# Kernel optimization log

Measured on AMD Instinct MI355X. Metric: run time of the kernel, lower is better.

## Reference

```python
import jax, jax.numpy as jnp
import numpy as np

NUM_TOKENS = 16384
DIM = 4096
N_EXPERTS = 256
ROUTE_SCALE = 1.0


def setup_inputs() -> dict:
    key = jax.random.key(0)
    k_x, k_w = jax.random.split(key)
    x = jax.random.normal(k_x, (NUM_TOKENS, DIM), dtype=jnp.float32)
    # nn.init.normal_(weight, std=0.02)
    weight = 0.02 * jax.random.normal(k_w, (N_EXPERTS, DIM), dtype=jnp.float32)
    return {"x": x, "weight": weight}


def reference(x, weight):
    # Router GEMM: [T, D] @ [D, E] -> [T, E]
    scores = jnp.einsum("td,ed->te", x, weight)
    # Eval-mode token_choice path: softmax in fp32
    probs = jax.nn.softmax(scores.astype(jnp.float32), axis=-1)  # [T, E]
    indices = jnp.argmax(probs, axis=-1, keepdims=True)  # [T, 1] int
    # Hard one-hot scatter of argmax
    y_hard = jax.nn.one_hot(indices[:, 0], N_EXPERTS, dtype=probs.dtype)  # [T, E]
    # Straight-through estimator mix
    ste = jax.lax.stop_gradient(y_hard - probs) + probs
    # Gather routing weight at the selected expert
    weights = jnp.take_along_axis(ste, indices, axis=-1)  # [T, 1]
    weights = (weights * ROUTE_SCALE).astype(x.dtype)
    return weights, indices
```

## Files before the change

### kernel.cpp

```cpp
#include <hip/hip_runtime.h>
#include <stdint.h>

#define NUM_TOKENS 16384
#define DIM        4096
#define NEXP       256
#define MB         32
#define BK         64
#define NITER      (DIM / BK)
#define APAD       72
#define NWAVES     8
#define MARGIN     0.025f
#define CAP        16384

typedef __attribute__((ext_vector_type(4))) float   f32x4;
typedef __attribute__((ext_vector_type(8))) __bf16  bf16x8;

static __device__ __forceinline__ unsigned short f32_to_bf16(float f) {
    unsigned int u = __float_as_uint(f);
    u += 0x7fffu + ((u >> 16) & 1u);
    return (unsigned short)(u >> 16);
}

__global__ void cvt_weights(const float* __restrict__ w,
                            unsigned short* __restrict__ wh,
                            int* __restrict__ counter) {
    if (blockIdx.x == 0 && threadIdx.x == 0) *counter = 0;
    const int n4 = NEXP * DIM / 4;
    const int stride = gridDim.x * blockDim.x;
    for (int i = blockIdx.x * blockDim.x + threadIdx.x; i < n4; i += stride) {
        float4 v = ((const float4*)w)[i];
        ushort4 h;
        h.x = f32_to_bf16(v.x); h.y = f32_to_bf16(v.y);
        h.z = f32_to_bf16(v.z); h.w = f32_to_bf16(v.w);
        ((ushort4*)wh)[i] = h;
    }
}

__global__ __launch_bounds__(512, 4) void gate_main(
    const float* __restrict__ x,
    const unsigned short* __restrict__ wh,
    float* __restrict__ out,
    int* __restrict__ counter,
    int4* __restrict__ entries)
{
    __shared__ unsigned short lAh[2][MB][APAD];
    __shared__ float4 cand[NWAVES][MB];

    const int tid  = threadIdx.x;
    const int wv   = tid >> 6;
    const int lane = tid & 63;
    const int tok0 = blockIdx.x * MB;

    const int ta   = tid >> 4;
    const int kcol = (tid & 15) * 4;
    const float* xrow = x + (size_t)(tok0 + ta) * DIM + kcol;

    const int quad = lane >> 4;
    const int col  = lane & 15;

    const unsigned short* bp[2];
    #pragma unroll
    for (int nt = 0; nt < 2; ++nt)
        bp[nt] = wh + (size_t)(wv * 32 + nt * 16 + col) * DIM + quad * 8;

    f32x4 acc[2][2];
    #pragma unroll
    for (int mt = 0; mt < 2; ++mt)
        #pragma unroll
        for (int nt = 0; nt < 2; ++nt)
            acc[mt][nt] = f32x4{0.f, 0.f, 0.f, 0.f};

    bf16x8 b[2][2];

    float4 xva = *(const float4*)(xrow);
    float4 xvb = *(const float4*)(xrow + BK);
    #pragma unroll
    for (int kk2 = 0; kk2 < 2; ++kk2)
        #pragma unroll
        for (int nt = 0; nt < 2; ++nt)
            b[kk2][nt] = *(const bf16x8*)(bp[nt] + kk2 * 32);
    {
        ushort4 h;
        h.x = f32_to_bf16(xva.x); h.y = f32_to_bf16(xva.y);
        h.z = f32_to_bf16(xva.z); h.w = f32_to_bf16(xva.w);
        *(ushort4*)&lAh[0][ta][kcol] = h;
    }
    xva = *(const float4*)(xrow + 2 * BK);

    asm volatile("s_waitcnt lgkmcnt(0)" ::: "memory");
    __builtin_amdgcn_s_barrier();
    asm volatile("" ::: "memory");

    auto iter_body = [&](int it, int cur, float4& xcons) {
        const int nxt = cur ^ 1;
        if (it + 1 < NITER) {
            ushort4 h;
            h.x = f32_to_bf16(xcons.x); h.y = f32_to_bf16(xcons.y);
            h.z = f32_to_bf16(xcons.z); h.w = f32_to_bf16(xcons.w);
            *(ushort4*)&lAh[nxt][ta][kcol] = h;
            if (it + 3 < NITER)
                xcons = *(const float4*)(xrow + (it + 3) * BK);
        }
        #pragma unroll
        for (int kk2 = 0; kk2 < 2; ++kk2) {
            bf16x8 ah0 = *(const bf16x8*)&lAh[cur][col][kk2 * 32 + quad * 8];
            bf16x8 ah1 = *(const bf16x8*)&lAh[cur][16 + col][kk2 * 32 + quad * 8];
            acc[0][0] = __builtin_amdgcn_mfma_f32_16x16x32_bf16(ah0, b[kk2][0], acc[0][0], 0, 0, 0);
            acc[1][0] = __builtin_amdgcn_mfma_f32_16x16x32_bf16(ah1, b[kk2][0], acc[1][0], 0, 0, 0);
            acc[0][1] = __builtin_amdgcn_mfma_f32_16x16x32_bf16(ah0, b[kk2][1], acc[0][1], 0, 0, 0);
            acc[1][1] = __builtin_amdgcn_mfma_f32_16x16x32_bf16(ah1, b[kk2][1], acc[1][1], 0, 0, 0);
            if (it + 1 < NITER) {
                #pragma unroll
                for (int nt = 0; nt < 2; ++nt)
                    b[kk2][nt] = *(const bf16x8*)(bp[nt] + (it + 1) * BK + kk2 * 32);
            }
        }
        asm volatile("s_waitcnt lgkmcnt(0)" ::: "memory");
        __builtin_amdgcn_s_barrier();
        asm volatile("" ::: "memory");
    };

    #pragma unroll 1
    for (int itp = 0; itp < NITER; itp += 2) {
        iter_body(itp,     0, xvb);
        iter_body(itp + 1, 1, xva);
    }

    #pragma unroll
    for (int mt = 0; mt < 2; ++mt) {
        #pragma unroll
        for (int r = 0; r < 4; ++r) {
            float s0 = acc[mt][0][r]; int e0 = wv * 32 + col;
            float s1 = acc[mt][1][r]; int e1 = e0 + 16;
            float t1s, t2s; int t1e, t2e;
            if (s1 > s0) { t1s = s1; t1e = e1; t2s = s0; t2e = e0; }
            else         { t1s = s0; t1e = e0; t2s = s1; t2e = e1; }
            #pragma unroll
            for (int m = 1; m <= 8; m <<= 1) {
                float o1s = __shfl_xor(t1s, m); int o1e = __shfl_xor(t1e, m);
                float o2s = __shfl_xor(t2s, m); int o2e = __shfl_xor(t2e, m);
                bool o1_top = (o1s > t1s) || (o1s == t1s && o1e < t1e);
                if (o1_top) {
                    bool keep_t1 = (t1s > o2s) || (t1s == o2s && t1e < o2e);
                    t2s = keep_t1 ? t1s : o2s; t2e = keep_t1 ? t1e : o2e;
                    t1s = o1s; t1e = o1e;
                } else {
                    bool o1_2nd = (o1s > t2s) || (o1s == t2s && o1e < t2e);
                    if (o1_2nd) { t2s = o1s; t2e = o1e; }
                }
            }
            if (col == 0) {
                int tok = mt * 16 + quad * 4 + r;
                cand[wv][tok] = make_float4(t1s, __int_as_float(t1e), t2s, __int_as_float(t2e));
            }
        }
    }
    __syncthreads();

    if (tid < MB) {
        float4 c0 = cand[0][tid];
        float t1s = c0.x; int t1e = __float_as_int(c0.y);
        float t2s = c0.z; int t2e = __float_as_int(c0.w);
        #pragma unroll
        for (int wvi = 1; wvi < NWAVES; ++wvi) {
            float4 c = cand[wvi][tid];
            float o1s = c.x; int o1e = __float_as_int(c.y);
            float o2s = c.z; int o2e = __float_as_int(c.w);
            bool o1_top = (o1s > t1s) || (o1s == t1s && o1e < t1e);
            if (o1_top) {
                bool keep_t1 = (t1s > o2s) || (t1s == o2s && t1e < o2e);
                t2s = keep_t1 ? t1s : o2s; t2e = keep_t1 ? t1e : o2e;
                t1s = o1s; t1e = o1e;
            } else {
                bool o1_2nd = (o1s > t2s) || (o1s == t2s && o1e < t2e);
                if (o1_2nd) { t2s = o1s; t2e = o1e; }
            }
        }
        const int gtok = tok0 + tid;
        out[gtok] = 1.0f;
        out[NUM_TOKENS + gtok] = (float)t1e;
        if (t1s - t2s < MARGIN) {
            int slot = atomicAdd(counter, 1);
            if (slot < CAP) entries[slot] = make_int4(gtok, t1e, t2e, 0);
        }
    }
}

__global__ void refine(const float* __restrict__ x,
                       const float* __restrict__ w,
                       const int* __restrict__ counter,
                       const int4* __restrict__ entries,
                       float* __restrict__ out) {
    const int gwave  = (blockIdx.x * blockDim.x + threadIdx.x) >> 6;
    const int lane   = threadIdx.x & 63;
    const int nwaves = (gridDim.x * blockDim.x) >> 6;
    int n = *counter; if (n > CAP) n = CAP;
    for (int i = gwave; i < n; i += nwaves) {
        int4 e = entries[i];
        const float* xr = x + (size_t)e.x * DIM;
        const float* w1 = w + (size_t)e.y * DIM;
        const float* w2 = w + (size_t)e.z * DIM;
        double d1 = 0.0, d2 = 0.0;
        for (int k = lane; k < DIM; k += 64) {
            double xv = (double)xr[k];
            d1 += xv * (double)w1[k];
            d2 += xv * (double)w2[k];
        }
        #pragma unroll
        for (int m = 32; m > 0; m >>= 1) {
            d1 += __shfl_xor(d1, m);
            d2 += __shfl_xor(d2, m);
        }
        if (lane == 0) {
            int best = (d1 > d2) ? e.y : ((d2 > d1) ? e.z : (e.y < e.z ? e.y : e.z));
            out[NUM_TOKENS + e.x] = (float)best;
        }
    }
}

extern "C" void kernel_launch(void* const* d_in, const int* in_sizes, int n_in,
                              void* d_out, int out_size, void* d_ws, size_t ws_size,
                              hipStream_t stream) {
    const float* x = (const float*)d_in[0];
    const float* w = (const float*)d_in[1];
    float* out = (float*)d_out;

    char* ws = (char*)d_ws;
    unsigned short* wh = (unsigned short*)ws;
    int*  counter = (int*)(ws + (2u << 20));
    int4* entries = (int4*)(ws + (2u << 20) + 16);

    cvt_weights<<<256, 256, 0, stream>>>(w, wh, counter);
    gate_main<<<NUM_TOKENS / MB, 512, 0, stream>>>(x, wh, out, counter, entries);
    refine<<<256, 256, 0, stream>>>(x, w, counter, entries, out);
}
```

Before: 456.4 us.

## Use 4 waves with 64 experts each and deepen x prefetch pipeline

```diff
diff --git a/kernel.cpp b/kernel.cpp
--- a/kernel.cpp
+++ b/kernel.cpp
@@ -8,12 +8,13 @@
 #define BK         64
 #define NITER      (DIM / BK)
 #define APAD       72
-#define NWAVES     8
+#define NWAVES     4
 #define MARGIN     0.025f
 #define CAP        16384
 
-typedef __attribute__((ext_vector_type(4))) float   f32x4;
-typedef __attribute__((ext_vector_type(8))) __bf16  bf16x8;
+typedef __attribute__((ext_vector_type(4))) float          f32x4;
+typedef __attribute__((ext_vector_type(8))) __bf16         bf16x8;
+typedef __attribute__((ext_vector_type(8))) unsigned short ushort8;
 
 static __device__ __forceinline__ unsigned short f32_to_bf16(float f) {
     unsigned int u = __float_as_uint(f);
@@ -36,14 +37,14 @@
     }
 }
 
-__global__ __launch_bounds__(512, 4) void gate_main(
+__global__ __launch_bounds__(256, 4) void gate_main(
     const float* __restrict__ x,
     const unsigned short* __restrict__ wh,
     float* __restrict__ out,
     int* __restrict__ counter,
     int4* __restrict__ entries)
 {
-    __shared__ unsigned short lAh[2][MB][APAD];
+    __shared__ unsigned short lAh[4][MB][APAD];
     __shared__ float4 cand[NWAVES][MB];
 
     const int tid  = threadIdx.x;
@@ -51,68 +52,74 @@
     const int lane = tid & 63;
     const int tok0 = blockIdx.x * MB;
 
-    const int ta   = tid >> 4;
-    const int kcol = (tid & 15) * 4;
-    const float* xrow = x + (size_t)(tok0 + ta) * DIM + kcol;
+    const int ta  = tid >> 3;
+    const int kc8 = (tid & 7) * 8;
+    const float* xrow = x + (size_t)(tok0 + ta) * DIM + kc8;
 
     const int quad = lane >> 4;
     const int col  = lane & 15;
 
-    const unsigned short* bp[2];
-    #pragma unroll
-    for (int nt = 0; nt < 2; ++nt)
-        bp[nt] = wh + (size_t)(wv * 32 + nt * 16 + col) * DIM + quad * 8;
-
-    f32x4 acc[2][2];
+    const int boff = (wv * 64 + col) * DIM + quad * 8;
+
+    f32x4 acc[2][4];
     #pragma unroll
     for (int mt = 0; mt < 2; ++mt)
         #pragma unroll
-        for (int nt = 0; nt < 2; ++nt)
+        for (int nt = 0; nt < 4; ++nt)
             acc[mt][nt] = f32x4{0.f, 0.f, 0.f, 0.f};
 
-    bf16x8 b[2][2];
-
-    float4 xva = *(const float4*)(xrow);
-    float4 xvb = *(const float4*)(xrow + BK);
+    bf16x8 b[2][4];
+
+    struct XQ { float4 lo, hi; };
+    auto cvt8 = [](const XQ& v) {
+        ushort8 h;
+        h[0] = f32_to_bf16(v.lo.x); h[1] = f32_to_bf16(v.lo.y);
+        h[2] = f32_to_bf16(v.lo.z); h[3] = f32_to_bf16(v.lo.w);
+        h[4] = f32_to_bf16(v.hi.x); h[5] = f32_to_bf16(v.hi.y);
+        h[6] = f32_to_bf16(v.hi.z); h[7] = f32_to_bf16(v.hi.w);
+        return h;
+    };
+    auto ldx = [&](int it) {
+        XQ v;
+        v.lo = *(const float4*)(xrow + it * BK);
+        v.hi = *(const float4*)(xrow + it * BK + 4);
+        return v;
+    };
+
+    XQ t0 = ldx(0), t1 = ldx(1);
+    XQ xq2 = ldx(2), xq3 = ldx(3), xq0 = ldx(4), xq1 = ldx(5);
     #pragma unroll
     for (int kk2 = 0; kk2 < 2; ++kk2)
         #pragma unroll
-        for (int nt = 0; nt < 2; ++nt)
-            b[kk2][nt] = *(const bf16x8*)(bp[nt] + kk2 * 32);
-    {
-        ushort4 h;
-        h.x = f32_to_bf16(xva.x); h.y = f32_to_bf16(xva.y);
-        h.z = f32_to_bf16(xva.z); h.w = f32_to_bf16(xva.w);
-        *(ushort4*)&lAh[0][ta][kcol] = h;
-    }
-    xva = *(const float4*)(xrow + 2 * BK);
-
+        for (int nt = 0; nt < 4; ++nt)
+            b[kk2][nt] = *(const bf16x8*)(wh + boff + nt * (16 * DIM) + kk2 * 32);
+    *(ushort8*)&lAh[0][ta][kc8] = cvt8(t0);
+    *(ushort8*)&lAh[1][ta][kc8] = cvt8(t1);
     asm volatile("s_waitcnt lgkmcnt(0)" ::: "memory");
     __builtin_amdgcn_s_barrier();
     asm volatile("" ::: "memory");
 
-    auto iter_body = [&](int it, int cur, float4& xcons) {
-        const int nxt = cur ^ 1;
-        if (it + 1 < NITER) {
-            ushort4 h;
-            h.x = f32_to_bf16(xcons.x); h.y = f32_to_bf16(xcons.y);
-            h.z = f32_to_bf16(xcons.z); h.w = f32_to_bf16(xcons.w);
-            *(ushort4*)&lAh[nxt][ta][kcol] = h;
-            if (it + 3 < NITER)
-                xcons = *(const float4*)(xrow + (it + 3) * BK);
-        }
+    auto body = [&](int it, XQ& xq) {
+        if (it + 2 < NITER) {
+            *(ushort8*)&lAh[(it + 2) & 3][ta][kc8] = cvt8(xq);
+            if (it + 6 < NITER)
+                xq = ldx(it + 6);
+        }
+        const int s = it & 3;
         #pragma unroll
         for (int kk2 = 0; kk2 < 2; ++kk2) {
-            bf16x8 ah0 = *(const bf16x8*)&lAh[cur][col][kk2 * 32 + quad * 8];
-            bf16x8 ah1 = *(const bf16x8*)&lAh[cur][16 + col][kk2 * 32 + quad * 8];
-            acc[0][0] = __builtin_amdgcn_mfma_f32_16x16x32_bf16(ah0, b[kk2][0], acc[0][0], 0, 0, 0);
-            acc[1][0] = __builtin_amdgcn_mfma_f32_16x16x32_bf16(ah1, b[kk2][0], acc[1][0], 0, 0, 0);
-            acc[0][1] = __builtin_amdgcn_mfma_f32_16x16x32_bf16(ah0, b[kk2][1], acc[0][1], 0, 0, 0);
-            acc[1][1] = __builtin_amdgcn_mfma_f32_16x16x32_bf16(ah1, b[kk2][1], acc[1][1], 0, 0, 0);
+            bf16x8 ah0 = *(const bf16x8*)&lAh[s][col][kk2 * 32 + quad * 8];
+            bf16x8 ah1 = *(const bf16x8*)&lAh[s][16 + col][kk2 * 32 + quad * 8];
+            #pragma unroll
+            for (int nt = 0; nt < 4; ++nt) {
+                acc[0][nt] = __builtin_amdgcn_mfma_f32_16x16x32_bf16(ah0, b[kk2][nt], acc[0][nt], 0, 0, 0);
+                acc[1][nt] = __builtin_amdgcn_mfma_f32_16x16x32_bf16(ah1, b[kk2][nt], acc[1][nt], 0, 0, 0);
+            }
             if (it + 1 < NITER) {
                 #pragma unroll
-                for (int nt = 0; nt < 2; ++nt)
-                    b[kk2][nt] = *(const bf16x8*)(bp[nt] + (it + 1) * BK + kk2 * 32);
+                for (int nt = 0; nt < 4; ++nt)
+                    b[kk2][nt] = *(const bf16x8*)(wh + boff + nt * (16 * DIM)
+                                                  + (it + 1) * BK + kk2 * 32);
             }
         }
         asm volatile("s_waitcnt lgkmcnt(0)" ::: "memory");
@@ -121,20 +128,28 @@
     };
 
     #pragma unroll 1
-    for (int itp = 0; itp < NITER; itp += 2) {
-        iter_body(itp,     0, xvb);
-        iter_body(itp + 1, 1, xva);
+    for (int itb = 0; itb < NITER; itb += 4) {
+        body(itb + 0, xq2);
+        body(itb + 1, xq3);
+        body(itb + 2, xq0);
+        body(itb + 3, xq1);
     }
 
     #pragma unroll
     for (int mt = 0; mt < 2; ++mt) {
         #pragma unroll
         for (int r = 0; r < 4; ++r) {
-            float s0 = acc[mt][0][r]; int e0 = wv * 32 + col;
-            float s1 = acc[mt][1][r]; int e1 = e0 + 16;
-            float t1s, t2s; int t1e, t2e;
-            if (s1 > s0) { t1s = s1; t1e = e1; t2s = s0; t2e = e0; }
-            else         { t1s = s0; t1e = e0; t2s = s1; t2e = e1; }
+            float t1s = acc[mt][0][r]; int t1e = wv * 64 + col;
+            float t2s = -__builtin_inff(); int t2e = 0x7fffffff;
+            #pragma unroll
+            for (int nt = 1; nt < 4; ++nt) {
+                float s = acc[mt][nt][r]; int e = wv * 64 + nt * 16 + col;
+                if (s > t1s) {
+                    t2s = t1s; t2e = t1e; t1s = s; t1e = e;
+                } else if (s > t2s || (s == t2s && e < t2e)) {
+                    t2s = s; t2e = e;
+                }
+            }
             #pragma unroll
             for (int m = 1; m <= 8; m <<= 1) {
                 float o1s = __shfl_xor(t1s, m); int o1e = __shfl_xor(t1e, m);
@@ -231,6 +246,6 @@
     int4* entries = (int4*)(ws + (2u << 20) + 16);
 
     cvt_weights<<<256, 256, 0, stream>>>(w, wh, counter);
-    gate_main<<<NUM_TOKENS / MB, 512, 0, stream>>>(x, wh, out, counter, entries);
+    gate_main<<<NUM_TOKENS / MB, 256, 0, stream>>>(x, wh, out, counter, entries);
     refine<<<256, 256, 0, stream>>>(x, w, counter, entries, out);
 }
```

Measured after the change: 482.7 us. +5.8%, slower.
